# Kernel optimization log

Hardware: AMD Instinct MI355X
Metric: run time of the kernel (lower is better)

The kernel has to match this reference:

```python
import jax, jax.numpy as jnp
import numpy as np

NUM_HEADS = 8
CHUNK = 64


def _retention(q, k, v):
    # q, k: (B, H, L, DK); v: (B, H, L, DV). Chunked linear retention with
    # per-head exponential decay gamma_h = 1 - 2^(-5-h) (RetNet convention).
    B, Hn, L, DK = q.shape
    DV = v.shape[-1]
    C = CHUNK
    N = L // C
    dt = q.dtype
    gamma = (1.0 - jnp.exp2(-5.0 - jnp.arange(Hn, dtype=jnp.float32))).astype(dt)  # (H,)
    q = q * (DK ** -0.5)
    idx = jnp.arange(C)
    diff = idx[:, None] - idx[None, :]
    # intra-chunk causal decay mask D[h,i,j] = gamma_h^(i-j) for i>=j else 0
    D = jnp.where(diff >= 0, gamma[:, None, None] ** diff, 0.0).astype(dt)      # (H,C,C)
    decay_q = (gamma[:, None] ** (idx[None, :] + 1)).astype(dt)                 # (H,C)
    decay_k = (gamma[:, None] ** (C - 1 - idx[None, :])).astype(dt)             # (H,C)
    decay_s = (gamma ** C).astype(dt)                                           # (H,)

    def to_chunks(x):
        return jnp.moveaxis(x.reshape(B, Hn, N, C, -1), 2, 0)  # (N,B,H,C,d)

    qs, ks, vs = map(to_chunks, (q, k, v))

    def step(S, x):
        qc, kc, vc = x  # (B,H,C,dk) / (B,H,C,dv)
        attn = jnp.einsum('bhid,bhjd->bhij', qc, kc) * D
        o_intra = jnp.einsum('bhij,bhje->bhie', attn, vc)
        o_inter = jnp.einsum('bhid,bhde->bhie', qc * decay_q[None, :, :, None], S)
        S_new = decay_s[None, :, None, None] * S + jnp.einsum(
            'bhjd,bhje->bhde', kc * decay_k[None, :, :, None], vc)
        return S_new, o_intra + o_inter

    S0 = jnp.zeros((B, Hn, DK, DV), dt)
    _, o = jax.lax.scan(step, S0, (qs, ks, vs))  # (N,B,H,C,DV)
    return jnp.moveaxis(o, 0, 2).reshape(B, Hn, L, DV)


def _xavier(key, fan_in, fan_out, gain=2 ** (-2.5)):
    limit = gain * np.sqrt(6.0 / (fan_in + fan_out))
    return jax.random.uniform(key, (fan_in, fan_out), jnp.float32, -limit, limit)


def setup_inputs() -> dict:
    key = jax.random.key(0)
    k0, k1, k2, k3, k4 = jax.random.split(key, 5)
    B, L, D = 2, 4096, 1024
    return {
        'hidden_states': jax.random.normal(k0, (B, L, D), jnp.float32),
        'rel_pos': jnp.zeros((1,), jnp.float32),  # unused by the module's forward
        'Wq': _xavier(k1, D, D),
        'Wk': _xavier(k2, D, D),
        'Wv': _xavier(k3, D, D),
        'Wo': _xavier(k4, D, D),
    }


def reference(hidden_states, rel_pos, Wq, Wk, Wv, Wo):
    B, L, Dm = hidden_states.shape
    Hd = Dm // NUM_HEADS
    q = (hidden_states @ Wq).reshape(B, L, NUM_HEADS, Hd).transpose(0, 2, 1, 3)
    k = (hidden_states @ Wk).reshape(B, L, NUM_HEADS, Hd).transpose(0, 2, 1, 3)
    v = (hidden_states @ Wv).reshape(B, L, NUM_HEADS, Hd).transpose(0, 2, 1, 3)
    o = _retention(q, k, v)  # (B,H,L,Hd)
    o = o.transpose(0, 2, 1, 3).reshape(B, L, Dm)
    return o @ Wo
```

## Files before the change

kernel.cpp:

```cpp
#include <hip/hip_runtime.h>
#include <hip/hip_bf16.h>

typedef __bf16 bf16;
typedef __bf16 bf16x8 __attribute__((ext_vector_type(8)));
typedef float f32x4 __attribute__((ext_vector_type(4)));

#define MFMA16(a, b, c) __builtin_amdgcn_mfma_f32_16x16x32_bf16((a), (b), (c), 0, 0, 0)


__global__ __launch_bounds__(256) void transpose_w(
    const float* __restrict__ Wq, const float* __restrict__ Wk,
    const float* __restrict__ Wv, const float* __restrict__ Wo,
    bf16* __restrict__ Wt) {
  __shared__ bf16 t[64 * 72];
  const float* src = (blockIdx.z == 0) ? Wq : (blockIdx.z == 1) ? Wk
                     : (blockIdx.z == 2) ? Wv : Wo;
  bf16* dst = Wt + (size_t)blockIdx.z * 1024 * 1024;
  const int k0 = blockIdx.x * 64, n0 = blockIdx.y * 64;
  const int tid = threadIdx.x;
#pragma unroll
  for (int s = 0; s < 4; ++s) {
    int u = tid + s * 256;
    int r = u >> 4, c4 = (u & 15) * 4;
    float4 f = *(const float4*)&src[(size_t)(k0 + r) * 1024 + n0 + c4];
    t[r * 72 + c4 + 0] = (bf16)f.x;
    t[r * 72 + c4 + 1] = (bf16)f.y;
    t[r * 72 + c4 + 2] = (bf16)f.z;
    t[r * 72 + c4 + 3] = (bf16)f.w;
  }
  __syncthreads();
#pragma unroll
  for (int s = 0; s < 2; ++s) {
    int u = tid + s * 256;
    int r = u >> 3, cc = u & 7;
    union { bf16 h[8]; uint4 u4; } pk;
#pragma unroll
    for (int j = 0; j < 8; ++j) pk.h[j] = t[(cc * 8 + j) * 72 + r];
    *(uint4*)&dst[(size_t)(n0 + r) * 1024 + k0 + cc * 8] = pk.u4;
  }
}

template <typename TA, typename TC>
__global__ __launch_bounds__(256) void gemm_bt(
    const TA* __restrict__ A, const bf16* __restrict__ Bt,
    TC* __restrict__ C, float alpha) {
  __shared__ bf16 lA[128 * 72];
  __shared__ bf16 lB[128 * 72];
  const int m0 = blockIdx.x * 128, n0 = blockIdx.y * 128;
  const int tid = threadIdx.x;
  const int w = tid >> 6, lane = tid & 63, lr = lane & 15, quad = lane >> 4;
  const int wm = w >> 1, wn = w & 1;
  f32x4 acc[4][4] = {};

  for (int it = 0; it < 16; ++it) {
    const int k0 = it * 64;
    if constexpr (sizeof(TA) == 4) {
#pragma unroll
      for (int s = 0; s < 8; ++s) {
        int u = tid + s * 256;
        int r = u >> 4, c4 = (u & 15) * 4;
        float4 f = *(const float4*)&A[(size_t)(m0 + r) * 1024 + k0 + c4];
        lA[r * 72 + c4 + 0] = (bf16)f.x;
        lA[r * 72 + c4 + 1] = (bf16)f.y;
        lA[r * 72 + c4 + 2] = (bf16)f.z;
        lA[r * 72 + c4 + 3] = (bf16)f.w;
      }
    } else {
#pragma unroll
      for (int s = 0; s < 4; ++s) {
        int u = tid + s * 256;
        int r = u >> 3, cc = u & 7;
        *(uint4*)&lA[r * 72 + cc * 8] =
            *(const uint4*)&A[(size_t)(m0 + r) * 1024 + k0 + cc * 8];
      }
    }
#pragma unroll
    for (int s = 0; s < 4; ++s) {
      int u = tid + s * 256;
      int r = u >> 3, cc = u & 7;
      *(uint4*)&lB[r * 72 + cc * 8] =
          *(const uint4*)&Bt[(size_t)(n0 + r) * 1024 + k0 + cc * 8];
    }
    __syncthreads();
#pragma unroll
    for (int kk = 0; kk < 2; ++kk) {
      bf16x8 af[4], bfv[4];
#pragma unroll
      for (int i = 0; i < 4; ++i)
        af[i] = *(bf16x8*)&lA[(wm * 64 + i * 16 + lr) * 72 + kk * 32 + quad * 8];
#pragma unroll
      for (int j = 0; j < 4; ++j)
        bfv[j] = *(bf16x8*)&lB[(wn * 64 + j * 16 + lr) * 72 + kk * 32 + quad * 8];
#pragma unroll
      for (int i = 0; i < 4; ++i)
#pragma unroll
        for (int j = 0; j < 4; ++j)
          acc[i][j] = MFMA16(af[i], bfv[j], acc[i][j]);
    }
    __syncthreads();
  }
#pragma unroll
  for (int i = 0; i < 4; ++i) {
#pragma unroll
    for (int j = 0; j < 4; ++j) {
      const int row = m0 + wm * 64 + i * 16 + quad * 4;
      const int col = n0 + wn * 64 + j * 16 + lr;
#pragma unroll
      for (int r = 0; r < 4; ++r)
        C[(size_t)(row + r) * 1024 + col] = (TC)(acc[i][j][r] * alpha);
    }
  }
}

__global__ __launch_bounds__(256) void chunk_kv(
    const bf16* __restrict__ kb, const bf16* __restrict__ vb,
    bf16* __restrict__ Tb) {
  __shared__ bf16 lK[128 * 72];
  __shared__ bf16 lV[128 * 72];
  const int g = blockIdx.x;
  const int bh = g >> 6, n = g & 63, b = bh >> 3, h = bh & 7;
  const float log2g = log2f(1.0f - exp2f(-5.0f - (float)h));
  const int tid = threadIdx.x;
  const size_t rowbase = (size_t)(b * 4096 + n * 64) * 1024 + h * 128;
  const bf16* kc = kb + rowbase;
  const bf16* vc = vb + rowbase;
#pragma unroll
  for (int s = 0; s < 4; ++s) {
    int u = tid + s * 256;
    int c = u >> 4, d0 = (u & 15) * 8;
    union { uint4 u4; bf16 h8[8]; } kv, vv;
    kv.u4 = *(const uint4*)&kc[(size_t)c * 1024 + d0];
    vv.u4 = *(const uint4*)&vc[(size_t)c * 1024 + d0];
    const float dec = exp2f((float)(63 - c) * log2g);
#pragma unroll
    for (int j = 0; j < 8; ++j) {
      lK[(d0 + j) * 72 + c] = (bf16)((float)kv.h8[j] * dec);
      lV[(d0 + j) * 72 + c] = vv.h8[j];
    }
  }
  __syncthreads();
  const int w = tid >> 6, lane = tid & 63, lr = lane & 15, quad = lane >> 4;
  const int wm = w >> 1, wn = w & 1;
  f32x4 acc[4][4] = {};
#pragma unroll
  for (int kk = 0; kk < 2; ++kk) {
    bf16x8 af[4], bv[4];
#pragma unroll
    for (int i = 0; i < 4; ++i)
      af[i] = *(bf16x8*)&lK[(wm * 64 + i * 16 + lr) * 72 + kk * 32 + quad * 8];
#pragma unroll
    for (int j = 0; j < 4; ++j)
      bv[j] = *(bf16x8*)&lV[(wn * 64 + j * 16 + lr) * 72 + kk * 32 + quad * 8];
#pragma unroll
    for (int i = 0; i < 4; ++i)
#pragma unroll
      for (int j = 0; j < 4; ++j)
        acc[i][j] = MFMA16(af[i], bv[j], acc[i][j]);
  }
  bf16* tchunk = Tb + (size_t)g * 16384;
#pragma unroll
  for (int i = 0; i < 4; ++i) {
#pragma unroll
    for (int j = 0; j < 4; ++j) {
      const int dk = wm * 64 + i * 16 + quad * 4;
      const int dv = wn * 64 + j * 16 + lr;
      union { bf16 h4[4]; uint2 u2; } pk;
#pragma unroll
      for (int r = 0; r < 4; ++r) pk.h4[r] = (bf16)acc[i][j][r];
      *(uint2*)&tchunk[(size_t)dv * 128 + dk] = pk.u2;
    }
  }
}

__global__ __launch_bounds__(256) void scan_state(bf16* __restrict__ Tb) {
  const int blk = blockIdx.x;
  const int bh = blk >> 6, seg = blk & 63, h = bh & 7;
  const float gs = exp2f(64.0f * log2f(1.0f - exp2f(-5.0f - (float)h)));
  const size_t base = (size_t)bh * 64 * 16384 + (size_t)seg * 256 + threadIdx.x;
  float S = 0.0f;
#pragma unroll 8
  for (int n = 0; n < 64; ++n) {
    const size_t a = base + (size_t)n * 16384;
    const float t = (float)Tb[a];
    Tb[a] = (bf16)S;
    S = gs * S + t;
  }
}

__global__ __launch_bounds__(256) void chunk_out(
    const bf16* __restrict__ qb, const bf16* __restrict__ kb,
    const bf16* __restrict__ vb, const bf16* __restrict__ Sp,
    bf16* __restrict__ ob) {
  __shared__ bf16 lQ[64 * 136];
  __shared__ bf16 lK[64 * 136];
  __shared__ bf16 lVt[128 * 72];
  __shared__ bf16 lP[64 * 72];
  const int g = blockIdx.x;
  const int bh = g >> 6, n = g & 63, b = bh >> 3, h = bh & 7;
  const float log2g = log2f(1.0f - exp2f(-5.0f - (float)h));
  const int tid = threadIdx.x;
  const size_t rowbase = (size_t)(b * 4096 + n * 64) * 1024 + h * 128;
  const bf16* qc = qb + rowbase;
  const bf16* kc = kb + rowbase;
  const bf16* vc = vb + rowbase;
#pragma unroll
  for (int s = 0; s < 4; ++s) {
    int u = tid + s * 256;
    int c = u >> 4, d0 = (u & 15) * 8;
    *(uint4*)&lQ[c * 136 + d0] = *(const uint4*)&qc[(size_t)c * 1024 + d0];
    *(uint4*)&lK[c * 136 + d0] = *(const uint4*)&kc[(size_t)c * 1024 + d0];
    union { uint4 u4; bf16 h8[8]; } vv;
    vv.u4 = *(const uint4*)&vc[(size_t)c * 1024 + d0];
#pragma unroll
    for (int j = 0; j < 8; ++j) lVt[(d0 + j) * 72 + c] = vv.h8[j];
  }
  __syncthreads();
  const int w = tid >> 6, lane = tid & 63, lr = lane & 15, quad = lane >> 4;

  f32x4 p[4] = {};
#pragma unroll
  for (int kk = 0; kk < 4; ++kk) {
    bf16x8 bfrag = *(bf16x8*)&lK[(w * 16 + lr) * 136 + kk * 32 + quad * 8];
#pragma unroll
    for (int i = 0; i < 4; ++i) {
      bf16x8 afrag = *(bf16x8*)&lQ[(i * 16 + lr) * 136 + kk * 32 + quad * 8];
      p[i] = MFMA16(afrag, bfrag, p[i]);
    }
  }
#pragma unroll
  for (int i = 0; i < 4; ++i) {
#pragma unroll
    for (int r = 0; r < 4; ++r) {
      const int row = i * 16 + quad * 4 + r;
      const int col = w * 16 + lr;
      const int diff = row - col;
      const float val =
          (diff >= 0) ? p[i][r] * exp2f((float)diff * log2g) : 0.0f;
      lP[row * 72 + col] = (bf16)val;
    }
  }
  __syncthreads();

  f32x4 oacc[4][2] = {};
#pragma unroll
  for (int j = 0; j < 2; ++j) {
    const int dvt = w * 32 + j * 16;
#pragma unroll
    for (int kk = 0; kk < 2; ++kk) {
      bf16x8 bfrag = *(bf16x8*)&lVt[(dvt + lr) * 72 + kk * 32 + quad * 8];
#pragma unroll
      for (int i = 0; i < 4; ++i) {
        bf16x8 afrag = *(bf16x8*)&lP[(i * 16 + lr) * 72 + kk * 32 + quad * 8];
        oacc[i][j] = MFMA16(afrag, bfrag, oacc[i][j]);
      }
    }
  }

  const bf16* sp = Sp + (size_t)g * 16384;
#pragma unroll
  for (int kk = 0; kk < 4; ++kk) {
    bf16x8 aN[4];
#pragma unroll
    for (int i = 0; i < 4; ++i) {
      bf16x8 a0 = *(bf16x8*)&lQ[(i * 16 + lr) * 136 + kk * 32 + quad * 8];
      const float dq = exp2f((float)(i * 16 + lr + 1) * log2g);
#pragma unroll
      for (int e = 0; e < 8; ++e) a0[e] = (bf16)((float)a0[e] * dq);
      aN[i] = a0;
    }
#pragma unroll
    for (int j = 0; j < 2; ++j) {
      bf16x8 bfrag =
          *(const bf16x8*)&sp[(size_t)(w * 32 + j * 16 + lr) * 128 + kk * 32 + quad * 8];
#pragma unroll
      for (int i = 0; i < 4; ++i) oacc[i][j] = MFMA16(aN[i], bfrag, oacc[i][j]);
    }
  }

  bf16* oc = ob + rowbase;
#pragma unroll
  for (int i = 0; i < 4; ++i)
#pragma unroll
    for (int j = 0; j < 2; ++j)
#pragma unroll
      for (int r = 0; r < 4; ++r) {
        const int row = i * 16 + quad * 4 + r;
        const int col = w * 32 + j * 16 + lr;
        oc[(size_t)row * 1024 + col] = (bf16)oacc[i][j][r];
      }
}

extern "C" void kernel_launch(void* const* d_in, const int* in_sizes, int n_in,
                              void* d_out, int out_size, void* d_ws,
                              size_t ws_size, hipStream_t stream) {
  const float* X  = (const float*)d_in[0];
  const float* Wq = (const float*)d_in[2];
  const float* Wk = (const float*)d_in[3];
  const float* Wv = (const float*)d_in[4];
  const float* Wo = (const float*)d_in[5];

  char* ws = (char*)d_ws;
  const size_t SZ_QKV = (size_t)8192 * 1024 * sizeof(bf16);
  bf16* qb = (bf16*)(ws);
  bf16* kb = (bf16*)(ws + SZ_QKV);
  bf16* vb = (bf16*)(ws + 2 * SZ_QKV);
  bf16* ob = (bf16*)(ws + 3 * SZ_QKV);
  bf16* Tb = (bf16*)(ws + 4 * SZ_QKV);
  bf16* Wt = (bf16*)(ws + 4 * SZ_QKV + (size_t)16 * 64 * 16384 * sizeof(bf16));

  transpose_w<<<dim3(16, 16, 4), 256, 0, stream>>>(Wq, Wk, Wv, Wo, Wt);

  const float qscale = 0.08838834764831845f;
  gemm_bt<float, bf16><<<dim3(64, 8), 256, 0, stream>>>(X, Wt, qb, qscale);
  gemm_bt<float, bf16><<<dim3(64, 8), 256, 0, stream>>>(X, Wt + (size_t)1 * 1024 * 1024, kb, 1.0f);
  gemm_bt<float, bf16><<<dim3(64, 8), 256, 0, stream>>>(X, Wt + (size_t)2 * 1024 * 1024, vb, 1.0f);

  chunk_kv<<<1024, 256, 0, stream>>>(kb, vb, Tb);
  scan_state<<<1024, 256, 0, stream>>>(Tb);
  chunk_out<<<1024, 256, 0, stream>>>(qb, kb, vb, Tb, ob);

  gemm_bt<bf16, float><<<dim3(64, 8), 256, 0, stream>>>(
      ob, Wt + (size_t)3 * 1024 * 1024, (float*)d_out, 1.0f);
}
```

Before: 259.2 us.

## Use direct global-to-LDS loads with XOR swizzle and batch QKV GEMMs

Converts the input activations to bf16 once in a separate kernel, so the GEMMs no longer convert fp32 on every tile load. The GEMM tile loads now use the global_load_lds builtin into an unpadded LDS layout with an XOR swizzle, which removes the VGPR round-trip and padding while aiming to avoid bank conflicts. The three Q/K/V projections are merged into one launch over a z grid dimension, giving more blocks in flight and fewer launches. The cost is an extra bf16 copy of X in workspace and a changed workspace layout.

```diff
diff --git a/kernel.cpp b/kernel.cpp
--- a/kernel.cpp
+++ b/kernel.cpp
@@ -7,6 +7,23 @@
 
 #define MFMA16(a, b, c) __builtin_amdgcn_mfma_f32_16x16x32_bf16((a), (b), (c), 0, 0, 0)
 
+
+__device__ __forceinline__ void g2l16(const bf16* g, bf16* l) {
+  __builtin_amdgcn_global_load_lds(
+      (const __attribute__((address_space(1))) void*)g,
+      (__attribute__((address_space(3))) void*)l, 16, 0, 0);
+}
+
+__global__ __launch_bounds__(256) void cvt_bf16(const float* __restrict__ X,
+                                                bf16* __restrict__ Y) {
+  const size_t i = ((size_t)blockIdx.x * 256 + threadIdx.x) * 8;
+  float4 a = *(const float4*)&X[i];
+  float4 b = *(const float4*)&X[i + 4];
+  union { bf16 h[8]; uint4 u; } p;
+  p.h[0] = (bf16)a.x; p.h[1] = (bf16)a.y; p.h[2] = (bf16)a.z; p.h[3] = (bf16)a.w;
+  p.h[4] = (bf16)b.x; p.h[5] = (bf16)b.y; p.h[6] = (bf16)b.z; p.h[7] = (bf16)b.w;
+  *(uint4*)&Y[i] = p.u;
+}
 
 __global__ __launch_bounds__(256) void transpose_w(
     const float* __restrict__ Wq, const float* __restrict__ Wk,
@@ -40,57 +57,50 @@
   }
 }
 
-template <typename TA, typename TC>
-__global__ __launch_bounds__(256) void gemm_bt(
-    const TA* __restrict__ A, const bf16* __restrict__ Bt,
+template <typename TC, int QKV>
+__global__ __launch_bounds__(256) void gemm_lds(
+    const bf16* __restrict__ A, const bf16* __restrict__ Bt,
     TC* __restrict__ C, float alpha) {
-  __shared__ bf16 lA[128 * 72];
-  __shared__ bf16 lB[128 * 72];
+  __shared__ bf16 lA[128 * 64];
+  __shared__ bf16 lB[128 * 64];
   const int m0 = blockIdx.x * 128, n0 = blockIdx.y * 128;
+  if (QKV) {
+    Bt += (size_t)blockIdx.z * 1024 * 1024;
+    C += (size_t)blockIdx.z * 8192 * 1024;
+    if (blockIdx.z != 0) alpha = 1.0f;
+  }
   const int tid = threadIdx.x;
   const int w = tid >> 6, lane = tid & 63, lr = lane & 15, quad = lane >> 4;
   const int wm = w >> 1, wn = w & 1;
+
+  const int srow = w * 32 + (lane >> 3);
+  const int clog = (lane & 7) ^ ((lane >> 3) & 7);
+  const bf16* gA = A + (size_t)(m0 + srow) * 1024 + clog * 8;
+  const bf16* gB = Bt + (size_t)(n0 + srow) * 1024 + clog * 8;
+
   f32x4 acc[4][4] = {};
 
   for (int it = 0; it < 16; ++it) {
     const int k0 = it * 64;
-    if constexpr (sizeof(TA) == 4) {
-#pragma unroll
-      for (int s = 0; s < 8; ++s) {
-        int u = tid + s * 256;
-        int r = u >> 4, c4 = (u & 15) * 4;
-        float4 f = *(const float4*)&A[(size_t)(m0 + r) * 1024 + k0 + c4];
-        lA[r * 72 + c4 + 0] = (bf16)f.x;
-        lA[r * 72 + c4 + 1] = (bf16)f.y;
-        lA[r * 72 + c4 + 2] = (bf16)f.z;
-        lA[r * 72 + c4 + 3] = (bf16)f.w;
-      }
-    } else {
-#pragma unroll
-      for (int s = 0; s < 4; ++s) {
-        int u = tid + s * 256;
-        int r = u >> 3, cc = u & 7;
-        *(uint4*)&lA[r * 72 + cc * 8] =
-            *(const uint4*)&A[(size_t)(m0 + r) * 1024 + k0 + cc * 8];
-      }
-    }
-#pragma unroll
-    for (int s = 0; s < 4; ++s) {
-      int u = tid + s * 256;
-      int r = u >> 3, cc = u & 7;
-      *(uint4*)&lB[r * 72 + cc * 8] =
-          *(const uint4*)&Bt[(size_t)(n0 + r) * 1024 + k0 + cc * 8];
+#pragma unroll
+    for (int is = 0; is < 4; ++is) {
+      g2l16(gA + (size_t)is * 8 * 1024 + k0, &lA[(w * 32 + is * 8) * 64]);
+      g2l16(gB + (size_t)is * 8 * 1024 + k0, &lB[(w * 32 + is * 8) * 64]);
     }
     __syncthreads();
 #pragma unroll
     for (int kk = 0; kk < 2; ++kk) {
       bf16x8 af[4], bfv[4];
 #pragma unroll
-      for (int i = 0; i < 4; ++i)
-        af[i] = *(bf16x8*)&lA[(wm * 64 + i * 16 + lr) * 72 + kk * 32 + quad * 8];
-#pragma unroll
-      for (int j = 0; j < 4; ++j)
-        bfv[j] = *(bf16x8*)&lB[(wn * 64 + j * 16 + lr) * 72 + kk * 32 + quad * 8];
+      for (int i = 0; i < 4; ++i) {
+        const int m = wm * 64 + i * 16 + lr;
+        af[i] = *(bf16x8*)&lA[m * 64 + (((kk * 4 + quad) ^ (lr & 7)) * 8)];
+      }
+#pragma unroll
+      for (int j = 0; j < 4; ++j) {
+        const int n = wn * 64 + j * 16 + lr;
+        bfv[j] = *(bf16x8*)&lB[n * 64 + (((kk * 4 + quad) ^ (lr & 7)) * 8)];
+      }
 #pragma unroll
       for (int i = 0; i < 4; ++i)
 #pragma unroll
@@ -302,23 +312,23 @@
   char* ws = (char*)d_ws;
   const size_t SZ_QKV = (size_t)8192 * 1024 * sizeof(bf16);
   bf16* qb = (bf16*)(ws);
-  bf16* kb = (bf16*)(ws + SZ_QKV);
-  bf16* vb = (bf16*)(ws + 2 * SZ_QKV);
   bf16* ob = (bf16*)(ws + 3 * SZ_QKV);
   bf16* Tb = (bf16*)(ws + 4 * SZ_QKV);
-  bf16* Wt = (bf16*)(ws + 4 * SZ_QKV + (size_t)16 * 64 * 16384 * sizeof(bf16));
-
+  bf16* Wt = (bf16*)(ws + 6 * SZ_QKV);
+  bf16* Xb = (bf16*)(ws + 6 * SZ_QKV + (size_t)4 * 1024 * 1024 * sizeof(bf16));
+  bf16* kb = qb + (size_t)8192 * 1024;
+  bf16* vb = kb + (size_t)8192 * 1024;
+
+  cvt_bf16<<<4096, 256, 0, stream>>>(X, Xb);
   transpose_w<<<dim3(16, 16, 4), 256, 0, stream>>>(Wq, Wk, Wv, Wo, Wt);
 
   const float qscale = 0.08838834764831845f;
-  gemm_bt<float, bf16><<<dim3(64, 8), 256, 0, stream>>>(X, Wt, qb, qscale);
-  gemm_bt<float, bf16><<<dim3(64, 8), 256, 0, stream>>>(X, Wt + (size_t)1 * 1024 * 1024, kb, 1.0f);
-  gemm_bt<float, bf16><<<dim3(64, 8), 256, 0, stream>>>(X, Wt + (size_t)2 * 1024 * 1024, vb, 1.0f);
+  gemm_lds<bf16, 1><<<dim3(64, 8, 3), 256, 0, stream>>>(Xb, Wt, qb, qscale);
 
   chunk_kv<<<1024, 256, 0, stream>>>(kb, vb, Tb);
   scan_state<<<1024, 256, 0, stream>>>(Tb);
   chunk_out<<<1024, 256, 0, stream>>>(qb, kb, vb, Tb, ob);
 
-  gemm_bt<bf16, float><<<dim3(64, 8), 256, 0, stream>>>(
+  gemm_lds<float, 0><<<dim3(64, 8), 256, 0, stream>>>(
       ob, Wt + (size_t)3 * 1024 * 1024, (float*)d_out, 1.0f);
 }
```

Result: faster. 232.4 us (-10.3%).
